# Optimization experiments

Hardware: AMD Instinct MI355X
Metric: run time of the kernel (lower is better)

Reference implementation:

```python
import jax, jax.numpy as jnp
import numpy as np

B, N, DIM, H, DH, MLP, DEPTH = 32, 256, 384, 6, 64, 1536, 12
INNER = H * DH
LN_EPS = 1e-5
LS_INIT = 0.1  # LayerScale init_eps for depth <= 18


def setup_inputs() -> dict:
    key = jax.random.key(0)
    ks = jax.random.split(key, 10)
    f = lambda k, shape, s=0.02: jax.random.normal(k, shape, jnp.float32) * s
    return {
        "x": jax.random.normal(ks[0], (B, N, DIM), jnp.float32),
        "ln1_g": jnp.ones((DEPTH, DIM), jnp.float32),
        "ln1_b": jnp.zeros((DEPTH, DIM), jnp.float32),
        "wq": f(ks[1], (DEPTH, DIM, INNER)),
        "wkv": f(ks[2], (DEPTH, DIM, 2 * INNER)),
        "scale": jnp.full((DEPTH, H), DH ** -0.5, jnp.float32),  # learned per-head scale
        "mix_pre": f(ks[3], (DEPTH, H, H), 1.0),   # torch.randn init
        "mix_post": f(ks[4], (DEPTH, H, H), 1.0),
        "wo": f(ks[5], (DEPTH, INNER, DIM)),
        "bo": jnp.zeros((DEPTH, DIM), jnp.float32),
        "ls1": jnp.full((DEPTH, DIM), LS_INIT, jnp.float32),
        "ln2_g": jnp.ones((DEPTH, DIM), jnp.float32),
        "ln2_b": jnp.zeros((DEPTH, DIM), jnp.float32),
        "w1": f(ks[6], (DEPTH, DIM, MLP)),
        "b1": jnp.zeros((DEPTH, MLP), jnp.float32),
        "w2": f(ks[7], (DEPTH, MLP, DIM)),
        "b2": jnp.zeros((DEPTH, DIM), jnp.float32),
        "ls2": jnp.full((DEPTH, DIM), LS_INIT, jnp.float32),
    }


def _layernorm(x, g, b):
    mu = jnp.mean(x, axis=-1, keepdims=True)
    var = jnp.mean(jnp.square(x - mu), axis=-1, keepdims=True)
    return (x - mu) * jax.lax.rsqrt(var + LN_EPS) * g + b


def reference(x, ln1_g, ln1_b, wq, wkv, scale, mix_pre, mix_post, wo, bo, ls1,
              ln2_g, ln2_b, w1, b1, w2, b2, ls2):
    diag = jnp.eye(N, dtype=bool)  # self-attention diagonal mask

    def block(x, p):
        (g1, bb1, wq_, wkv_, sc, mp, mq, wo_, bo_, l1,
         g2, bb2, w1_, b1_, w2_, b2_, l2) = p
        # --- talking-heads attention (PreNorm + LayerScale + residual) ---
        y = _layernorm(x, g1, bb1)
        q = (y @ wq_).reshape(B, N, H, DH).transpose(0, 2, 1, 3)       # b h n d
        kv = y @ wkv_
        k, v = jnp.split(kv, 2, axis=-1)
        k = k.reshape(B, N, H, DH).transpose(0, 2, 1, 3)
        v = v.reshape(B, N, H, DH).transpose(0, 2, 1, 3)
        dots = jnp.einsum('bhid,bhjd->bhij', q, k) * sc[None, :, None, None]
        dots = jnp.einsum('bhij,hg->bgij', dots, mp)                   # pre-softmax head mix
        dots = jnp.where(diag, -jnp.inf, dots)                         # mask self positions
        attn = jax.nn.softmax(dots, axis=-1)
        attn = jnp.einsum('bhij,hg->bgij', attn, mq)                   # post-softmax head mix
        o = jnp.einsum('bhij,bhjd->bhid', attn, v)
        o = o.transpose(0, 2, 1, 3).reshape(B, N, INNER) @ wo_ + bo_
        x = o * l1 + x
        # --- FFN (PreNorm + LayerScale + residual) ---
        y2 = _layernorm(x, g2, bb2)
        h = jax.nn.gelu(y2 @ w1_ + b1_, approximate=False)
        x = (h @ w2_ + b2_) * l2 + x
        return x, None

    params = (ln1_g, ln1_b, wq, wkv, scale, mix_pre, mix_post, wo, bo, ls1,
              ln2_g, ln2_b, w1, b1, w2, b2, ls2)
    x, _ = jax.lax.scan(block, x, params)
    return x
```

## Files before the change

kernel.cpp:

```cpp
#include <hip/hip_runtime.h>
#include <hip/hip_bf16.h>
#include <math.h>

#define B_ 32
#define N_ 256
#define DIM_ 384
#define H_ 6
#define DH_ 64
#define INNER_ 384
#define MLP_ 1536
#define DEPTH_ 12
#define T_ (B_ * N_)

typedef __bf16 bf16x8 __attribute__((ext_vector_type(8)));
typedef __bf16 bf16x4 __attribute__((ext_vector_type(4)));
typedef float f32x4 __attribute__((ext_vector_type(4)));

typedef const __attribute__((address_space(1))) void* gas_ptr;
typedef __attribute__((address_space(3))) void* las_ptr;

#define WQKV_OFF 0
#define WO_OFF   (1152 * 384)
#define W1_OFF   (WO_OFF + 384 * 384)
#define W2_OFF   (W1_OFF + 1536 * 384)
#define WBUF_ELEMS (W2_OFF + 384 * 1536)

__global__ __launch_bounds__(256) void convert_w_all(
    const float* __restrict__ wq0, const float* __restrict__ wkv0,
    const float* __restrict__ wo0, const float* __restrict__ w10,
    const float* __restrict__ w20, __bf16* __restrict__ wbuf0)
{
    __shared__ float til[64][65];
    int t = blockIdx.x;
    int l = t / 432; t -= l * 432;
    const float* wq  = wq0  + (size_t)l * DIM_ * INNER_;
    const float* wkv = wkv0 + (size_t)l * DIM_ * 2 * INNER_;
    const float* wo  = wo0  + (size_t)l * INNER_ * DIM_;
    const float* w1  = w10  + (size_t)l * DIM_ * MLP_;
    const float* w2  = w20  + (size_t)l * MLP_ * DIM_;
    __bf16* wbuf = wbuf0 + (size_t)l * WBUF_ELEMS;

    int lane = threadIdx.x & 63, seg = threadIdx.x >> 6;
    const float* src; __bf16* dst;
    int Ns, sc, dK, dR, k0;
    if (t < 108) {
        int nt = t / 6, kt = t % 6;
        int n0 = nt * 64; k0 = kt * 64;
        dst = wbuf + WQKV_OFF; dK = 384; dR = n0;
        if (n0 < 384) { src = wq;  Ns = 384; sc = n0; }
        else          { src = wkv; Ns = 768; sc = n0 - 384; }
    } else if (t < 144) {
        int u = t - 108; int nt = u / 6, kt = u % 6;
        src = wo; Ns = 384; sc = nt * 64;
        dst = wbuf + WO_OFF; dK = 384; dR = nt * 64; k0 = kt * 64;
    } else if (t < 288) {
        int u = t - 144; int nt = u / 6, kt = u % 6;
        src = w1; Ns = 1536; sc = nt * 64;
        dst = wbuf + W1_OFF; dK = 384; dR = nt * 64; k0 = kt * 64;
    } else {
        int u = t - 288; int nt = u / 24, kt = u % 24;
        src = w2; Ns = 384; sc = nt * 64;
        dst = wbuf + W2_OFF; dK = 1536; dR = nt * 64; k0 = kt * 64;
    }
    #pragma unroll
    for (int r = 0; r < 16; ++r) {
        int i = seg * 16 + r;
        til[i][lane] = src[(size_t)(k0 + i) * Ns + sc + lane];
    }
    __syncthreads();
    #pragma unroll
    for (int r = 0; r < 16; ++r) {
        int i = seg * 16 + r;
        dst[(size_t)(dR + i) * dK + k0 + lane] = (__bf16)til[lane][i];
    }
}

__global__ __launch_bounds__(256) void ln1w(
    const float* __restrict__ x, const float* __restrict__ g,
    const float* __restrict__ b, __bf16* __restrict__ y)
{
    size_t row = blockIdx.x * 4 + (threadIdx.x >> 6);
    int lane = threadIdx.x & 63;
    const float* xr = x + row * DIM_;
    float v[6];
    #pragma unroll
    for (int s = 0; s < 6; ++s) v[s] = xr[lane + 64 * s];
    float sum = 0.f;
    #pragma unroll
    for (int s = 0; s < 6; ++s) sum += v[s];
    #pragma unroll
    for (int o = 32; o > 0; o >>= 1) sum += __shfl_xor(sum, o);
    float mu = sum * (1.0f / DIM_);
    float var = 0.f;
    #pragma unroll
    for (int s = 0; s < 6; ++s) { float d = v[s] - mu; var += d * d; }
    #pragma unroll
    for (int o = 32; o > 0; o >>= 1) var += __shfl_xor(var, o);
    float rs = rsqrtf(var * (1.0f / DIM_) + 1e-5f);
    __bf16* yr = y + row * DIM_;
    #pragma unroll
    for (int s = 0; s < 6; ++s) {
        int e = lane + 64 * s;
        yr[e] = (__bf16)((v[s] - mu) * rs * g[e] + b[e]);
    }
}

template<int MODE, int K, int BM, int BN, int BK, int NT>
__global__ __launch_bounds__(256) void gemmt(
    const __bf16* __restrict__ A, const __bf16* __restrict__ Bt,
    const float* __restrict__ bias, const float* __restrict__ ls,
    float* __restrict__ xf, __bf16* __restrict__ out,
    __bf16* __restrict__ oq, __bf16* __restrict__ ok, __bf16* __restrict__ ov,
    int Nn)
{
    constexpr int WM = BM / 32, WN = BN / 32;
    constexpr int KS = BK / 32;
    constexpr int MT = T_ / BM;
    constexpr int nIter = K / BK;
    constexpr bool SWZ = (BK == 64);
    constexpr int RPI = 512 / BK;
    constexpr int CL  = BK / 8;
    constexpr int LPT = BM / (4 * RPI) + BN / (4 * RPI);
    static_assert(LPT == 4 || LPT == 6, "vmcnt literal must match LPT");

    __shared__ __align__(16) __bf16 sA[2][BM * BK];
    __shared__ __align__(16) __bf16 sB[2][BN * BK];

    int id = blockIdx.x;
    constexpr int nxg = (MT * NT) / 8;
    int wg = (id & 7) * nxg + (id >> 3);
    int bm = (wg / NT) * BM;
    int bn = (wg % NT) * BN;
    int tid = threadIdx.x;
    int lane = tid & 63, wid = tid >> 6;
    int wm = (wid & 1) * (BM / 2), wn = (wid >> 1) * (BN / 2);
    int fm = lane & 15, fq = lane >> 4;

    f32x4 acc[WM][WN] = {};

    int lr = lane / CL, lc = lane % CL;
    int lcs = SWZ ? (lc ^ lr) : lc;
    const __bf16* aBase = A + (size_t)(bm + wid * RPI + lr) * K + lcs * 8;
    const __bf16* bBase = Bt + (size_t)(bn + wid * RPI + lr) * K + lcs * 8;

    auto stage = [&](int buf, int kk) {
        #pragma unroll
        for (int qI = 0; qI < BM / (4 * RPI); ++qI)
            __builtin_amdgcn_global_load_lds(
                (gas_ptr)(aBase + (size_t)(qI * 4 * RPI) * K + kk),
                (las_ptr)&sA[buf][qI * 2048 + wid * 512], 16, 0, 0);
        #pragma unroll
        for (int qI = 0; qI < BN / (4 * RPI); ++qI)
            __builtin_amdgcn_global_load_lds(
                (gas_ptr)(bBase + (size_t)(qI * 4 * RPI) * K + kk),
                (las_ptr)&sB[buf][qI * 2048 + wid * 512], 16, 0, 0);
    };

    stage(0, 0);

    #pragma unroll
    for (int i = 0; i < nIter; ++i) {
        int cur = i & 1;
        if (i + 1 < nIter) {
            stage(cur ^ 1, (i + 1) * BK);
            if constexpr (LPT == 4)
                asm volatile("s_waitcnt vmcnt(4)" ::: "memory");
            else
                asm volatile("s_waitcnt vmcnt(6)" ::: "memory");
        } else {
            asm volatile("s_waitcnt vmcnt(0)" ::: "memory");
        }
        __builtin_amdgcn_s_barrier();
        __builtin_amdgcn_sched_barrier(0);

        bf16x8 af[KS][WM], bfr[KS][WN];
        #pragma unroll
        for (int ks = 0; ks < KS; ++ks) {
            #pragma unroll
            for (int ii = 0; ii < WM; ++ii) {
                int row = wm + ii * 16 + fm;
                int c = SWZ ? (((ks * 4 + fq) ^ (row & 7)) * 8) : (ks * 32 + fq * 8);
                af[ks][ii] = *(const bf16x8*)&sA[cur][row * BK + c];
            }
            #pragma unroll
            for (int jj = 0; jj < WN; ++jj) {
                int row = wn + jj * 16 + fm;
                int c = SWZ ? (((ks * 4 + fq) ^ (row & 7)) * 8) : (ks * 32 + fq * 8);
                bfr[ks][jj] = *(const bf16x8*)&sB[cur][row * BK + c];
            }
        }
        #pragma unroll
        for (int ks = 0; ks < KS; ++ks)
            #pragma unroll
            for (int ii = 0; ii < WM; ++ii)
                #pragma unroll
                for (int jj = 0; jj < WN; ++jj)
                    acc[ii][jj] = __builtin_amdgcn_mfma_f32_16x16x32_bf16(
                        af[ks][ii], bfr[ks][jj], acc[ii][jj], 0, 0, 0);

        if (i + 1 < nIter) {
            asm volatile("s_waitcnt lgkmcnt(0)" ::: "memory");
            __builtin_amdgcn_sched_barrier(0);
            __builtin_amdgcn_s_barrier();
            __builtin_amdgcn_sched_barrier(0);
        }
    }

    #pragma unroll
    for (int jj = 0; jj < WN; ++jj) {
        int col = bn + wn + jj * 16 + fm;
        float bv = (MODE != 0) ? bias[col] : 0.0f;
        float lv = (MODE == 2) ? ls[col] : 0.0f;
        #pragma unroll
        for (int ii = 0; ii < WM; ++ii) {
            #pragma unroll
            for (int r = 0; r < 4; ++r) {
                int row = bm + wm + ii * 16 + fq * 4 + r;
                float v = acc[ii][jj][r];
                if (MODE == 0) {
                    if (col < 384)      oq[(size_t)row * 384 + col] = (__bf16)v;
                    else if (col < 768) ok[(size_t)row * 384 + col - 384] = (__bf16)v;
                    else {
                        int bb = row >> 8, tj = row & 255;
                        ov[((size_t)bb * 384 + (col - 768)) * 256 + tj] = (__bf16)v;
                    }
                } else if (MODE == 1) {
                    v += bv;
                    v = 0.5f * v * (1.0f + erff(v * 0.70710678118f));
                    out[(size_t)row * Nn + col] = (__bf16)v;
                } else {
                    size_t idx = (size_t)row * Nn + col;
                    xf[idx] = (v + bv) * lv + xf[idx];
                }
            }
        }
    }
}

#define PAD_S 264

__global__ __launch_bounds__(384) void attn_mfma(
    const __bf16* __restrict__ q, const __bf16* __restrict__ kb,
    const __bf16* __restrict__ vT, const float* __restrict__ scale,
    const float* __restrict__ mp, const float* __restrict__ mq,
    __bf16* __restrict__ o)
{
    __shared__ __bf16 sbuf[96][PAD_S];

    int id = blockIdx.x;
    int b = (id & 7) + ((id >> 3) & 3) * 8;
    int i0 = (id >> 5) * 16;
    int tid = threadIdx.x;
    int lane = tid & 63, wid = tid >> 6;
    int fm = lane & 15, fq = lane >> 4;

    int h = wid;
    bf16x8 qf[2];
    #pragma unroll
    for (int ks = 0; ks < 2; ++ks)
        qf[ks] = *(const bf16x8*)&q[(size_t)(b * 256 + i0 + fm) * 384 + h * 64 + ks * 32 + fq * 8];
    #pragma unroll 4
    for (int jt = 0; jt < 16; ++jt) {
        f32x4 a = {};
        #pragma unroll
        for (int ks = 0; ks < 2; ++ks) {
            bf16x8 bfr = *(const bf16x8*)&kb[(size_t)(b * 256 + jt * 16 + fm) * 384 + h * 64 + ks * 32 + fq * 8];
            a = __builtin_amdgcn_mfma_f32_16x16x32_bf16(qf[ks], bfr, a, 0, 0, 0);
        }
        #pragma unroll
        for (int r = 0; r < 4; ++r)
            sbuf[h * 16 + fq * 4 + r][jt * 16 + fm] = (__bf16)a[r];
    }

    float mps[36], mqs[36];
    #pragma unroll
    for (int t = 0; t < 36; ++t) { mps[t] = mp[t] * scale[t / 6]; mqs[t] = mq[t]; }

    __syncthreads();

    for (int i = wid; i < 16; i += 6) {
        float sv[6][4];
        #pragma unroll
        for (int h2 = 0; h2 < 6; ++h2) {
            bf16x4 v4 = *(const bf16x4*)&sbuf[h2 * 16 + i][lane * 4];
            #pragma unroll
            for (int c = 0; c < 4; ++c) sv[h2][c] = (float)v4[c];
        }
        int drow = i0 + i;
        float pv[6][4];
        #pragma unroll
        for (int g2 = 0; g2 < 6; ++g2) {
            float t0[4];
            #pragma unroll
            for (int c = 0; c < 4; ++c) {
                float r2 = 0.f;
                #pragma unroll
                for (int h2 = 0; h2 < 6; ++h2) r2 += sv[h2][c] * mps[h2 * 6 + g2];
                t0[c] = (lane * 4 + c == drow) ? -1e30f : r2;
            }
            float m = fmaxf(fmaxf(t0[0], t0[1]), fmaxf(t0[2], t0[3]));
            #pragma unroll
            for (int off = 32; off > 0; off >>= 1) m = fmaxf(m, __shfl_xor(m, off));
            float e0 = __expf(t0[0] - m), e1 = __expf(t0[1] - m);
            float e2 = __expf(t0[2] - m), e3 = __expf(t0[3] - m);
            float s = e0 + e1 + e2 + e3;
            #pragma unroll
            for (int off = 32; off > 0; off >>= 1) s += __shfl_xor(s, off);
            float inv = 1.0f / s;
            pv[g2][0] = e0 * inv; pv[g2][1] = e1 * inv;
            pv[g2][2] = e2 * inv; pv[g2][3] = e3 * inv;
        }
        #pragma unroll
        for (int g2 = 0; g2 < 6; ++g2) {
            bf16x4 w4;
            #pragma unroll
            for (int c = 0; c < 4; ++c) {
                float r2 = 0.f;
                #pragma unroll
                for (int h2 = 0; h2 < 6; ++h2) r2 += pv[h2][c] * mqs[h2 * 6 + g2];
                w4[c] = (__bf16)r2;
            }
            *(bf16x4*)&sbuf[g2 * 16 + i][lane * 4] = w4;
        }
    }
    __syncthreads();

    int gg = wid;
    f32x4 acco[4] = {};
    #pragma unroll
    for (int jc = 0; jc < 4; ++jc) {
        #pragma unroll
        for (int ks = 0; ks < 2; ++ks) {
            bf16x8 af = *(const bf16x8*)&sbuf[gg * 16 + fm][jc * 64 + ks * 32 + fq * 8];
            #pragma unroll
            for (int nt = 0; nt < 4; ++nt) {
                bf16x8 bfr = *(const bf16x8*)&vT[(size_t)(b * 384 + gg * 64 + nt * 16 + fm) * 256 + jc * 64 + ks * 32 + fq * 8];
                acco[nt] = __builtin_amdgcn_mfma_f32_16x16x32_bf16(af, bfr, acco[nt], 0, 0, 0);
            }
        }
    }
    #pragma unroll
    for (int nt = 0; nt < 4; ++nt)
        #pragma unroll
        for (int r = 0; r < 4; ++r)
            o[(size_t)(b * 256 + i0 + fq * 4 + r) * 384 + gg * 64 + nt * 16 + fm] = (__bf16)acco[nt][r];
}

extern "C" void kernel_launch(void* const* d_in, const int* in_sizes, int n_in,
                              void* d_out, int out_size, void* d_ws, size_t ws_size,
                              hipStream_t stream) {
    const float* x      = (const float*)d_in[0];
    const float* ln1_g  = (const float*)d_in[1];
    const float* ln1_b  = (const float*)d_in[2];
    const float* wq     = (const float*)d_in[3];
    const float* wkv    = (const float*)d_in[4];
    const float* scale  = (const float*)d_in[5];
    const float* mixp   = (const float*)d_in[6];
    const float* mixq   = (const float*)d_in[7];
    const float* wo     = (const float*)d_in[8];
    const float* bo     = (const float*)d_in[9];
    const float* ls1    = (const float*)d_in[10];
    const float* ln2_g  = (const float*)d_in[11];
    const float* ln2_b  = (const float*)d_in[12];
    const float* w1     = (const float*)d_in[13];
    const float* b1     = (const float*)d_in[14];
    const float* w2     = (const float*)d_in[15];
    const float* b2     = (const float*)d_in[16];
    const float* ls2    = (const float*)d_in[17];

    char* ws = (char*)d_ws;
    float*  xf = (float*)ws;                      ws += (size_t)T_ * DIM_ * 4;
    __bf16* y  = (__bf16*)ws;                     ws += (size_t)T_ * DIM_ * 2;
    __bf16* q  = (__bf16*)ws;                     ws += (size_t)T_ * DIM_ * 2;
    __bf16* kb = (__bf16*)ws;                     ws += (size_t)T_ * DIM_ * 2;
    __bf16* vT = (__bf16*)ws;                     ws += (size_t)T_ * DIM_ * 2;
    __bf16* o  = (__bf16*)ws;                     ws += (size_t)T_ * DIM_ * 2;
    __bf16* wbuf = (__bf16*)ws;                   ws += (size_t)WBUF_ELEMS * DEPTH_ * 2;
    __bf16* h  = q;

    size_t nBytes = (size_t)T_ * DIM_ * sizeof(float);
    hipMemcpyAsync(xf, x, nBytes, hipMemcpyDeviceToDevice, stream);

    convert_w_all<<<432 * DEPTH_, 256, 0, stream>>>(wq, wkv, wo, w1, w2, wbuf);

    for (int l = 0; l < DEPTH_; ++l) {
        __bf16* wl = wbuf + (size_t)l * WBUF_ELEMS;

        ln1w<<<T_ / 4, 256, 0, stream>>>(xf, ln1_g + (size_t)l * DIM_, ln1_b + (size_t)l * DIM_, y);

        gemmt<0, 384, 128, 128, 32, 9><<<576, 256, 0, stream>>>(
            y, wl + WQKV_OFF, nullptr, nullptr, nullptr, nullptr,
            q, kb, vT, 1152);

        attn_mfma<<<512, 384, 0, stream>>>(
            q, kb, vT, scale + (size_t)l * H_,
            mixp + (size_t)l * H_ * H_, mixq + (size_t)l * H_ * H_, o);

        gemmt<2, 384, 64, 64, 64, 6><<<768, 256, 0, stream>>>(
            o, wl + WO_OFF, bo + (size_t)l * DIM_, ls1 + (size_t)l * DIM_,
            xf, nullptr, nullptr, nullptr, nullptr, DIM_);

        ln1w<<<T_ / 4, 256, 0, stream>>>(xf, ln2_g + (size_t)l * DIM_, ln2_b + (size_t)l * DIM_, y);

        gemmt<1, 384, 128, 256, 32, 6><<<384, 256, 0, stream>>>(
            y, wl + W1_OFF, b1 + (size_t)l * MLP_, nullptr,
            nullptr, h, nullptr, nullptr, nullptr, MLP_);

        gemmt<2, 1536, 64, 64, 64, 6><<<768, 256, 0, stream>>>(
            h, wl + W2_OFF, b2 + (size_t)l * DIM_, ls2 + (size_t)l * DIM_,
            xf, nullptr, nullptr, nullptr, nullptr, DIM_);
    }

    hipMemcpyAsync(d_out, xf, nBytes, hipMemcpyDeviceToDevice, stream);
}
```

Baseline: 1.704 ms.

## Stream B weight fragments directly into registers for QKV and FFN1 GEMMs

Adds a STREAMB path to the GEMM in which each wave loads its B (weight) MFMA fragments straight from global memory into double-buffered registers, skipping LDS staging for B. Only A is staged through LDS. The QKV and FFN1 GEMMs use this path, and FFN1 also moves from a 128x256 tile to 128x128 with twice as many blocks. The aim is to cut LDS traffic and footprint and raise occupancy, at the cost of more global/L2 reads of weights (no reuse across waves) and more register pressure.

Measured after the change: 1.812 ms. 6.4% more time.

```diff
diff --git a/kernel.cpp b/kernel.cpp
--- a/kernel.cpp
+++ b/kernel.cpp
@@ -105,7 +105,7 @@
     }
 }
 
-template<int MODE, int K, int BM, int BN, int BK, int NT>
+template<int MODE, int K, int BM, int BN, int BK, int NT, bool STREAMB = false>
 __global__ __launch_bounds__(256) void gemmt(
     const __bf16* __restrict__ A, const __bf16* __restrict__ Bt,
     const float* __restrict__ bias, const float* __restrict__ ls,
@@ -120,11 +120,10 @@
     constexpr bool SWZ = (BK == 64);
     constexpr int RPI = 512 / BK;
     constexpr int CL  = BK / 8;
-    constexpr int LPT = BM / (4 * RPI) + BN / (4 * RPI);
-    static_assert(LPT == 4 || LPT == 6, "vmcnt literal must match LPT");
+    static_assert(!STREAMB || (BK == 32 && BM == 128 && BN == 128), "STREAMB mapping");
 
     __shared__ __align__(16) __bf16 sA[2][BM * BK];
-    __shared__ __align__(16) __bf16 sB[2][BN * BK];
+    __shared__ __align__(16) __bf16 sB[STREAMB ? 1 : 2][STREAMB ? 16 : BN * BK];
 
     int id = blockIdx.x;
     constexpr int nxg = (MT * NT) / 8;
@@ -143,66 +142,114 @@
     const __bf16* aBase = A + (size_t)(bm + wid * RPI + lr) * K + lcs * 8;
     const __bf16* bBase = Bt + (size_t)(bn + wid * RPI + lr) * K + lcs * 8;
 
-    auto stage = [&](int buf, int kk) {
+    auto stageA = [&](int buf, int kk) {
         #pragma unroll
         for (int qI = 0; qI < BM / (4 * RPI); ++qI)
             __builtin_amdgcn_global_load_lds(
                 (gas_ptr)(aBase + (size_t)(qI * 4 * RPI) * K + kk),
                 (las_ptr)&sA[buf][qI * 2048 + wid * 512], 16, 0, 0);
-        #pragma unroll
-        for (int qI = 0; qI < BN / (4 * RPI); ++qI)
-            __builtin_amdgcn_global_load_lds(
-                (gas_ptr)(bBase + (size_t)(qI * 4 * RPI) * K + kk),
-                (las_ptr)&sB[buf][qI * 2048 + wid * 512], 16, 0, 0);
     };
-
-    stage(0, 0);
-
-    #pragma unroll
-    for (int i = 0; i < nIter; ++i) {
-        int cur = i & 1;
-        if (i + 1 < nIter) {
-            stage(cur ^ 1, (i + 1) * BK);
-            if constexpr (LPT == 4)
-                asm volatile("s_waitcnt vmcnt(4)" ::: "memory");
-            else
+    auto stageB = [&](int buf, int kk) {
+        if constexpr (!STREAMB) {
+            #pragma unroll
+            for (int qI = 0; qI < BN / (4 * RPI); ++qI)
+                __builtin_amdgcn_global_load_lds(
+                    (gas_ptr)(bBase + (size_t)(qI * 4 * RPI) * K + kk),
+                    (las_ptr)&sB[buf][qI * 2048 + wid * 512], 16, 0, 0);
+        }
+    };
+
+    if constexpr (STREAMB) {
+        const __bf16* bFrag = Bt + (size_t)(bn + wn + fm) * K + fq * 8;
+        bf16x8 breg[2][WN];
+        auto loadB = [&](int set, int kk) {
+            #pragma unroll
+            for (int jj = 0; jj < WN; ++jj)
+                breg[set][jj] = *(const bf16x8*)(bFrag + (size_t)(jj * 16) * K + kk);
+        };
+
+        stageA(0, 0); loadB(0, 0);
+
+        #pragma unroll
+        for (int i = 0; i < nIter; ++i) {
+            int cur = i & 1;
+            if (i + 1 < nIter) {
+                stageA(cur ^ 1, (i + 1) * BK);
+                loadB(cur ^ 1, (i + 1) * BK);
                 asm volatile("s_waitcnt vmcnt(6)" ::: "memory");
-        } else {
-            asm volatile("s_waitcnt vmcnt(0)" ::: "memory");
-        }
-        __builtin_amdgcn_s_barrier();
-        __builtin_amdgcn_sched_barrier(0);
-
-        bf16x8 af[KS][WM], bfr[KS][WN];
-        #pragma unroll
-        for (int ks = 0; ks < KS; ++ks) {
-            #pragma unroll
-            for (int ii = 0; ii < WM; ++ii) {
-                int row = wm + ii * 16 + fm;
-                int c = SWZ ? (((ks * 4 + fq) ^ (row & 7)) * 8) : (ks * 32 + fq * 8);
-                af[ks][ii] = *(const bf16x8*)&sA[cur][row * BK + c];
-            }
-            #pragma unroll
-            for (int jj = 0; jj < WN; ++jj) {
-                int row = wn + jj * 16 + fm;
-                int c = SWZ ? (((ks * 4 + fq) ^ (row & 7)) * 8) : (ks * 32 + fq * 8);
-                bfr[ks][jj] = *(const bf16x8*)&sB[cur][row * BK + c];
-            }
-        }
-        #pragma unroll
-        for (int ks = 0; ks < KS; ++ks)
+            } else {
+                asm volatile("s_waitcnt vmcnt(0)" ::: "memory");
+            }
+            __builtin_amdgcn_s_barrier();
+            __builtin_amdgcn_sched_barrier(0);
+
+            bf16x8 af[WM];
+            #pragma unroll
+            for (int ii = 0; ii < WM; ++ii)
+                af[ii] = *(const bf16x8*)&sA[cur][(wm + ii * 16 + fm) * BK + fq * 8];
             #pragma unroll
             for (int ii = 0; ii < WM; ++ii)
                 #pragma unroll
                 for (int jj = 0; jj < WN; ++jj)
                     acc[ii][jj] = __builtin_amdgcn_mfma_f32_16x16x32_bf16(
-                        af[ks][ii], bfr[ks][jj], acc[ii][jj], 0, 0, 0);
-
-        if (i + 1 < nIter) {
-            asm volatile("s_waitcnt lgkmcnt(0)" ::: "memory");
-            __builtin_amdgcn_sched_barrier(0);
+                        af[ii], breg[cur][jj], acc[ii][jj], 0, 0, 0);
+
+            if (i + 1 < nIter) {
+                asm volatile("s_waitcnt lgkmcnt(0)" ::: "memory");
+                __builtin_amdgcn_sched_barrier(0);
+                __builtin_amdgcn_s_barrier();
+                __builtin_amdgcn_sched_barrier(0);
+            }
+        }
+    } else {
+        constexpr int LPT = BM / (4 * RPI) + BN / (4 * RPI);
+        static_assert(LPT == 4, "vmcnt literal assumes 4 loads per tile per wave");
+        stageA(0, 0); stageB(0, 0);
+
+        #pragma unroll
+        for (int i = 0; i < nIter; ++i) {
+            int cur = i & 1;
+            if (i + 1 < nIter) {
+                stageA(cur ^ 1, (i + 1) * BK);
+                stageB(cur ^ 1, (i + 1) * BK);
+                asm volatile("s_waitcnt vmcnt(4)" ::: "memory");
+            } else {
+                asm volatile("s_waitcnt vmcnt(0)" ::: "memory");
+            }
             __builtin_amdgcn_s_barrier();
             __builtin_amdgcn_sched_barrier(0);
+
+            bf16x8 af[KS][WM], bfr[KS][WN];
+            #pragma unroll
+            for (int ks = 0; ks < KS; ++ks) {
+                #pragma unroll
+                for (int ii = 0; ii < WM; ++ii) {
+                    int row = wm + ii * 16 + fm;
+                    int c = SWZ ? (((ks * 4 + fq) ^ (row & 7)) * 8) : (ks * 32 + fq * 8);
+                    af[ks][ii] = *(const bf16x8*)&sA[cur][row * BK + c];
+                }
+                #pragma unroll
+                for (int jj = 0; jj < WN; ++jj) {
+                    int row = wn + jj * 16 + fm;
+                    int c = SWZ ? (((ks * 4 + fq) ^ (row & 7)) * 8) : (ks * 32 + fq * 8);
+                    bfr[ks][jj] = *(const bf16x8*)&sB[cur][row * BK + c];
+                }
+            }
+            #pragma unroll
+            for (int ks = 0; ks < KS; ++ks)
+                #pragma unroll
+                for (int ii = 0; ii < WM; ++ii)
+                    #pragma unroll
+                    for (int jj = 0; jj < WN; ++jj)
+                        acc[ii][jj] = __builtin_amdgcn_mfma_f32_16x16x32_bf16(
+                            af[ks][ii], bfr[ks][jj], acc[ii][jj], 0, 0, 0);
+
+            if (i + 1 < nIter) {
+                asm volatile("s_waitcnt lgkmcnt(0)" ::: "memory");
+                __builtin_amdgcn_sched_barrier(0);
+                __builtin_amdgcn_s_barrier();
+                __builtin_amdgcn_sched_barrier(0);
+            }
         }
     }
 
@@ -388,7 +435,7 @@
 
         ln1w<<<T_ / 4, 256, 0, stream>>>(xf, ln1_g + (size_t)l * DIM_, ln1_b + (size_t)l * DIM_, y);
 
-        gemmt<0, 384, 128, 128, 32, 9><<<576, 256, 0, stream>>>(
+        gemmt<0, 384, 128, 128, 32, 9, true><<<576, 256, 0, stream>>>(
             y, wl + WQKV_OFF, nullptr, nullptr, nullptr, nullptr,
             q, kb, vT, 1152);
 
@@ -402,7 +449,7 @@
 
         ln1w<<<T_ / 4, 256, 0, stream>>>(xf, ln2_g + (size_t)l * DIM_, ln2_b + (size_t)l * DIM_, y);
 
-        gemmt<1, 384, 128, 256, 32, 6><<<384, 256, 0, stream>>>(
+        gemmt<1, 384, 128, 128, 32, 12, true><<<768, 256, 0, stream>>>(
             y, wl + W1_OFF, b1 + (size_t)l * MLP_, nullptr,
             nullptr, h, nullptr, nullptr, nullptr, MLP_);
 
```
